# Kernel tuning notes

Hardware: AMD Instinct MI355X
Metric: run time of the kernel (lower is better)

## Reference

```python
import jax, jax.numpy as jnp
import numpy as np

HIDDEN = 1024
HEADS = 16
HEAD_DIM = 64
B, S = 4, 2048


def setup_inputs() -> dict:
    key = jax.random.key(0)
    ks = jax.random.split(key, 7)
    sd = 1.0 / np.sqrt(HIDDEN)
    inp = {
        "inputs": jax.random.normal(ks[0], (B, S, HIDDEN), dtype=jnp.float32),
        "Wq": jax.random.normal(ks[1], (HIDDEN, HEADS * HEAD_DIM), dtype=jnp.float32) * sd,
        "bq": jnp.zeros((HEADS * HEAD_DIM,), dtype=jnp.float32),
        "Wk": jax.random.normal(ks[2], (HIDDEN, HEADS * HEAD_DIM), dtype=jnp.float32) * sd,
        "bk": jnp.zeros((HEADS * HEAD_DIM,), dtype=jnp.float32),
        "Wv": jax.random.normal(ks[3], (HIDDEN, HEADS * HEAD_DIM), dtype=jnp.float32) * sd,
        "bv": jnp.zeros((HEADS * HEAD_DIM,), dtype=jnp.float32),
        "attention_mask": jnp.zeros((B, 1, 1, S), dtype=jnp.float32),
        "attention_head_size": HEAD_DIM,
    }
    return inp


def _rope_tables(seq_len, head_dim, dtype):
    # embeddings[n, d] with interleaved sin/cos layout: [s0, c0, s1, c1, ...]
    pos = jnp.arange(seq_len, dtype=jnp.float32)
    inv_freq = jnp.power(10000.0, -2.0 * jnp.arange(head_dim // 2, dtype=jnp.float32) / head_dim)
    ang = pos[:, None] * inv_freq[None, :]                      # [S, D/2]
    emb = jnp.stack([jnp.sin(ang), jnp.cos(ang)], axis=-1).reshape(seq_len, head_dim)
    cos_pos = jnp.repeat(emb[:, 1::2], 2, axis=-1).astype(dtype)  # [S, D]
    sin_pos = jnp.repeat(emb[:, 0::2], 2, axis=-1).astype(dtype)  # [S, D]
    return cos_pos[None, None], sin_pos[None, None]               # [1,1,S,D]


def _rotate(x):
    # stack([-x_odd, x_even], -1).reshape: interleaved rotate-half
    x2 = jnp.stack([-x[..., 1::2], x[..., 0::2]], axis=-1)
    return x2.reshape(x.shape)


def reference(inputs, Wq, bq, Wk, bk, Wv, bv, attention_mask, attention_head_size):
    Bq, Sq, _ = inputs.shape
    H = HEADS
    D = attention_head_size
    all_head = H * D

    def proj(W, b):
        y = inputs @ W + b                              # [B,S,H*D]
        return y.reshape(Bq, Sq, H, D).transpose(0, 2, 1, 3)  # [B,H,S,D]

    q = proj(Wq, bq)
    k = proj(Wk, bk)
    v = proj(Wv, bv)

    cos_pos, sin_pos = _rope_tables(Sq, D, inputs.dtype)
    q = q * cos_pos + _rotate(q) * sin_pos
    k = k * cos_pos + _rotate(k) * sin_pos

    # NOTE: module scales by sqrt(all_head_size), not sqrt(head_dim)
    scores = jnp.einsum("bhqd,bhkd->bhqk", q, k) / jnp.sqrt(jnp.float32(all_head)).astype(inputs.dtype)
    scores = scores + attention_mask
    probs = jax.nn.softmax(scores, axis=-1)
    ctx = jnp.einsum("bhqk,bhkd->bhqd", probs, v)       # [B,H,S,D]
    ctx = ctx.transpose(0, 2, 1, 3).reshape(Bq, Sq, all_head)
    return ctx, q, k
```

## Files before the change

kernel.cpp:

```cpp
#include <hip/hip_runtime.h>


#define B_  4
#define S_  2048
#define H_  16
#define D_  64
#define HID 1024
#define M_  (B_ * S_)

typedef __attribute__((ext_vector_type(8))) short    bf16x8;
typedef __attribute__((ext_vector_type(4))) float    f32x4;
typedef __attribute__((ext_vector_type(4))) unsigned short u16x4;
typedef __attribute__((ext_vector_type(8))) unsigned short u16x8;
typedef __attribute__((ext_vector_type(2))) unsigned u32x2;

__device__ __forceinline__ unsigned short f2bf(float f) {
    union { float f; unsigned u; } v; v.f = f;
    unsigned r = v.u + 0x7fffu + ((v.u >> 16) & 1u);
    return (unsigned short)(r >> 16);
}

__device__ __forceinline__ void async16(const unsigned short* g, unsigned short* l) {
    __builtin_amdgcn_global_load_lds(
        (const __attribute__((address_space(1))) void*)g,
        (__attribute__((address_space(3))) void*)l, 16, 0, 0);
}

__global__ __launch_bounds__(256) void rope_table_kernel(float* __restrict__ tab)
{
    int i = blockIdx.x * 256 + threadIdx.x;
    int s = i >> 6, d = i & 63;
    const float NEG_LN1E4_32 = -0.28782313662425576f;
    float freq = __expf(NEG_LN1E4_32 * (float)(d >> 1));
    float ang = (float)s * freq;
    tab[i]          = cosf(ang);
    tab[131072 + i] = sinf(ang);
}

__global__ __launch_bounds__(256) void cast_x_kernel(
    const float* __restrict__ X, unsigned short* __restrict__ Xb)
{
    int i = (blockIdx.x * 256 + threadIdx.x) * 4;
    float4 v = *(const float4*)(X + i);
    u16x4 o;
    o[0] = f2bf(v.x); o[1] = f2bf(v.y); o[2] = f2bf(v.z); o[3] = f2bf(v.w);
    *(u16x4*)(Xb + i) = o;
}

__global__ __launch_bounds__(256) void cast_wt_kernel(
    const float* __restrict__ Wq, const float* __restrict__ Wk,
    const float* __restrict__ Wv, unsigned short* __restrict__ Wt)
{
    __shared__ float tile[64][65];
    int z = blockIdx.z;
    const float* W = (z == 0) ? Wq : ((z == 1) ? Wk : Wv);
    unsigned short* out = Wt + (size_t)z * HID * HID;
    int n0 = blockIdx.x * 64, k0 = blockIdx.y * 64;
    int tx = threadIdx.x & 63, ty0 = threadIdx.x >> 6;
#pragma unroll
    for (int i = 0; i < 16; i++) {
        int ty = ty0 * 16 + i;
        tile[ty][tx] = W[(size_t)(k0 + ty) * HID + n0 + tx];
    }
    __syncthreads();
#pragma unroll
    for (int i = 0; i < 16; i++) {
        int ty = ty0 * 16 + i;
        out[(size_t)(n0 + ty) * HID + k0 + tx] = f2bf(tile[tx][ty]);
    }
}

#define BM 128
#define BN 128
#define BKQ 32

__global__ __launch_bounds__(256) void qkv_gemm_kernel(
    const unsigned short* __restrict__ Xb, const unsigned short* __restrict__ Wt,
    const float* __restrict__ bq, const float* __restrict__ bk,
    const float* __restrict__ bv,
    const float* __restrict__ cosT, const float* __restrict__ sinT,
    float* out,
    unsigned short* __restrict__ Qb, unsigned short* __restrict__ Kb,
    unsigned short* __restrict__ Vb)
{
    __shared__ unsigned short As[BM * BKQ];
    __shared__ unsigned short Bs[BN * BKQ];

    const size_t Q_OFF = (size_t)B_ * S_ * HID;
    const size_t K_OFF = 2 * Q_OFF;

    int z = blockIdx.z;
    const unsigned short* W = Wt + (size_t)z * HID * HID;
    const float* bias = (z == 0) ? bq : ((z == 1) ? bk : bv);

    int n0 = blockIdx.x * BN, m0 = blockIdx.y * BM;
    int tid = threadIdx.x;
    int wave = tid >> 6, lane = tid & 63;
    int quad = lane >> 4, l15 = lane & 15;
    int wm = (wave >> 1) * 64;
    int wn = (wave & 1) * 64;

    const unsigned short* Ag = Xb + (size_t)m0 * HID;
    const unsigned short* Bg = W  + (size_t)n0 * HID;

    int e0 = tid, e1 = 256 + tid;
    int r0 = e0 >> 2, c0 = (e0 & 3) * 8;
    int r1 = e1 >> 2, c1 = (e1 & 3) * 8;

    f32x4 acc[4][4] = {};

    for (int k0 = 0; k0 < HID; k0 += BKQ) {
        async16(Ag + (size_t)r0 * HID + k0 + c0, &As[e0 * 8]);
        async16(Ag + (size_t)r1 * HID + k0 + c1, &As[e1 * 8]);
        async16(Bg + (size_t)r0 * HID + k0 + c0, &Bs[e0 * 8]);
        async16(Bg + (size_t)r1 * HID + k0 + c1, &Bs[e1 * 8]);
        __syncthreads();

        bf16x8 af[4], bf[4];
#pragma unroll
        for (int t = 0; t < 4; t++)
            af[t] = *(const bf16x8*)&As[(wm + t * 16 + l15) * BKQ + quad * 8];
#pragma unroll
        for (int t = 0; t < 4; t++)
            bf[t] = *(const bf16x8*)&Bs[(wn + t * 16 + l15) * BKQ + quad * 8];
#pragma unroll
        for (int rt = 0; rt < 4; rt++)
#pragma unroll
            for (int ct = 0; ct < 4; ct++)
                acc[rt][ct] = __builtin_amdgcn_mfma_f32_16x16x32_bf16(
                    af[rt], bf[ct], acc[rt][ct], 0, 0, 0);
        __syncthreads();
    }

#pragma unroll
    for (int ct = 0; ct < 4; ct++) {
        int n = n0 + wn + ct * 16 + l15;
        float bval = bias[n];
        int h = n >> 6, d = n & 63;
#pragma unroll
        for (int rt = 0; rt < 4; rt++) {
#pragma unroll
            for (int r = 0; r < 4; r++) {
                int m = m0 + wm + rt * 16 + quad * 4 + r;
                int b = m >> 11, s = m & (S_ - 1);
                float y = acc[rt][ct][r] + bval;
                size_t o = ((size_t)(b * H_ + h) * S_ + s) * D_ + d;
                if (z < 2) {
                    float c  = cosT[s * 64 + d];
                    float sn = sinT[s * 64 + d];
                    float p = __shfl_xor(y, 1);
                    float yr = ((d & 1) == 0) ? (y * c - p * sn) : (y * c + p * sn);
                    if (z == 0) { out[Q_OFF + o] = yr; Qb[o] = f2bf(yr); }
                    else        { out[K_OFF + o] = yr; Kb[o] = f2bf(yr); }
                } else {
                    Vb[o] = f2bf(y);
                }
            }
        }
    }
}

__global__ __launch_bounds__(256) void transpose_v_kernel(
    const unsigned short* __restrict__ Vb, unsigned short* __restrict__ Vt)
{
    __shared__ unsigned short t[64][72];
    int bh = blockIdx.y;
    int s0 = blockIdx.x * 64;
    const unsigned short* src = Vb + ((size_t)bh * S_ + s0) * D_;
    unsigned short* dst = Vt + (size_t)bh * D_ * S_;
    int tid = threadIdx.x;
#pragma unroll
    for (int i = 0; i < 2; i++) {
        int e = i * 256 + tid;
        int row = e >> 3, c = (e & 7) * 8;
        u16x8 v = *(const u16x8*)(src + (size_t)row * D_ + c);
#pragma unroll
        for (int j = 0; j < 8; j++) t[row][c + j] = v[j];
    }
    __syncthreads();
#pragma unroll
    for (int i = 0; i < 2; i++) {
        int e = i * 256 + tid;
        int d = e >> 3, sc = (e & 7) * 8;
        u16x8 v;
#pragma unroll
        for (int j = 0; j < 8; j++) v[j] = t[sc + j][d];
        *(u16x8*)(dst + (size_t)d * S_ + s0 + sc) = v;
    }
}

#define TR 72

__global__ __launch_bounds__(256, 4) void attn_kernel(
    const unsigned short* __restrict__ Qb, const unsigned short* __restrict__ Kb,
    const unsigned short* __restrict__ Vt, const float* __restrict__ mask,
    float* __restrict__ out)
{
    __shared__ union {
        struct {
            unsigned short Ks[2][64 * TR];
            unsigned short Vs[2][64 * TR];
        } s;
        float oT[4][2][16][68];
    } u;

    int h  = blockIdx.x;
    int qt = blockIdx.y;
    int b  = blockIdx.z;
    int tid = threadIdx.x;
    int wave = tid >> 6, lane = tid & 63;
    int quad = lane >> 4, l15 = lane & 15;

    size_t bh = (size_t)(b * H_ + h);
    const unsigned short* Qp = Qb + bh * S_ * D_;
    const unsigned short* Kp = Kb + bh * S_ * D_;
    const unsigned short* Vp = Vt + bh * D_ * S_;
    const float* mp = mask + (size_t)b * S_;

    bf16x8 qb[2][2];
#pragma unroll
    for (int qg = 0; qg < 2; qg++)
#pragma unroll
        for (int hf = 0; hf < 2; hf++) {
            int qrow = qt * 128 + qg * 64 + wave * 16 + l15;
            qb[qg][hf] = *(const bf16x8*)(Qp + (size_t)qrow * D_ + hf * 32 + quad * 8);
        }

    f32x4 o[2][4] = {};
    float psum[2] = {0.0f, 0.0f};
    const float C2    = 0.03125f * 1.44269504f;
    const float LOG2E = 1.44269504f;

    int sr0 = tid >> 3, sg0 = (tid & 7) * 8;
    int sr1 = sr0 + 32;

    u16x8 kr0 = *(const u16x8*)(Kp + (size_t)sr0 * D_ + sg0);
    u16x8 kr1 = *(const u16x8*)(Kp + (size_t)sr1 * D_ + sg0);
    u16x8 vr0 = *(const u16x8*)(Vp + (size_t)sr0 * S_ + sg0);
    u16x8 vr1 = *(const u16x8*)(Vp + (size_t)sr1 * S_ + sg0);

    int cur = 0;
    for (int kv0 = 0; kv0 < S_; kv0 += 64) {
        *(u16x8*)&u.s.Ks[cur][sr0 * TR + sg0] = kr0;
        *(u16x8*)&u.s.Ks[cur][sr1 * TR + sg0] = kr1;
        *(u16x8*)&u.s.Vs[cur][sr0 * TR + sg0] = vr0;
        *(u16x8*)&u.s.Vs[cur][sr1 * TR + sg0] = vr1;
        __syncthreads();

        int kvn = (kv0 + 64 < S_) ? kv0 + 64 : 0;
        kr0 = *(const u16x8*)(Kp + (size_t)(kvn + sr0) * D_ + sg0);
        kr1 = *(const u16x8*)(Kp + (size_t)(kvn + sr1) * D_ + sg0);
        vr0 = *(const u16x8*)(Vp + (size_t)sr0 * S_ + kvn + sg0);
        vr1 = *(const u16x8*)(Vp + (size_t)sr1 * S_ + kvn + sg0);

        const unsigned short* Ksc = u.s.Ks[cur];
        const unsigned short* Vsc = u.s.Vs[cur];

        f32x4 sa[2][4] = {};
        __builtin_amdgcn_s_setprio(1);
#pragma unroll
        for (int mt = 0; mt < 4; mt++) {
            bf16x8 kf0 = *(const bf16x8*)&Ksc[(mt * 16 + l15) * TR + quad * 8];
            bf16x8 kf1 = *(const bf16x8*)&Ksc[(mt * 16 + l15) * TR + 32 + quad * 8];
#pragma unroll
            for (int qg = 0; qg < 2; qg++) {
                sa[qg][mt] = __builtin_amdgcn_mfma_f32_16x16x32_bf16(kf0, qb[qg][0], sa[qg][mt], 0, 0, 0);
                sa[qg][mt] = __builtin_amdgcn_mfma_f32_16x16x32_bf16(kf1, qb[qg][1], sa[qg][mt], 0, 0, 0);
            }
        }
        __builtin_amdgcn_s_setprio(0);

        unsigned pw[2][4][2];
#pragma unroll
        for (int mt = 0; mt < 4; mt++) {
            f32x4 mkv = *(const f32x4*)(mp + kv0 + mt * 16 + quad * 4);
#pragma unroll
            for (int qg = 0; qg < 2; qg++) {
                f32x4 pv;
#pragma unroll
                for (int r = 0; r < 4; r++)
                    pv[r] = exp2f(sa[qg][mt][r] * C2 + mkv[r] * LOG2E);
                psum[qg] += (pv[0] + pv[1]) + (pv[2] + pv[3]);
                asm("v_cvt_pk_bf16_f32 %0, %1, %2"
                    : "=v"(pw[qg][mt][0]) : "v"(pv[0]), "v"(pv[1]));
                asm("v_cvt_pk_bf16_f32 %0, %1, %2"
                    : "=v"(pw[qg][mt][1]) : "v"(pv[2]), "v"(pv[3]));
            }
        }

        bf16x8 pb[2][2];
#pragma unroll
        for (int qg = 0; qg < 2; qg++)
#pragma unroll
            for (int hf = 0; hf < 2; hf++) {
                union { unsigned w[4]; bf16x8 v; } pbu;
#pragma unroll
                for (int t = 0; t < 2; t++) {
                    unsigned A = pw[qg][2 * hf + 0][t];
                    unsigned B = pw[qg][2 * hf + 1][t];
                    u32x2 r1 = __builtin_amdgcn_permlane32_swap(A, B, false, false);
                    u32x2 r2 = __builtin_amdgcn_permlane16_swap(r1[0], r1[1], false, false);
                    pbu.w[t]     = r2[0];
                    pbu.w[2 + t] = r2[1];
                }
                pb[qg][hf] = pbu.v;
            }

        __builtin_amdgcn_s_setprio(1);
#pragma unroll
        for (int ct = 0; ct < 4; ct++) {
            bf16x8 vf0 = *(const bf16x8*)&Vsc[(ct * 16 + l15) * TR + quad * 8];
            bf16x8 vf1 = *(const bf16x8*)&Vsc[(ct * 16 + l15) * TR + 32 + quad * 8];
#pragma unroll
            for (int qg = 0; qg < 2; qg++) {
                o[qg][ct] = __builtin_amdgcn_mfma_f32_16x16x32_bf16(vf0, pb[qg][0], o[qg][ct], 0, 0, 0);
                o[qg][ct] = __builtin_amdgcn_mfma_f32_16x16x32_bf16(vf1, pb[qg][1], o[qg][ct], 0, 0, 0);
            }
        }
        __builtin_amdgcn_s_setprio(0);

        cur ^= 1;
    }
    __syncthreads();

#pragma unroll
    for (int qg = 0; qg < 2; qg++) {
        psum[qg] += __shfl_xor(psum[qg], 16);
        psum[qg] += __shfl_xor(psum[qg], 32);
    }

#pragma unroll
    for (int qg = 0; qg < 2; qg++) {
        float inv = 1.0f / psum[qg];
#pragma unroll
        for (int ct = 0; ct < 4; ct++) {
            float4 vv;
            vv.x = o[qg][ct][0] * inv; vv.y = o[qg][ct][1] * inv;
            vv.z = o[qg][ct][2] * inv; vv.w = o[qg][ct][3] * inv;
            *(float4*)&u.oT[wave][qg][l15][ct * 16 + quad * 4] = vv;
        }
    }
    __builtin_amdgcn_wave_barrier();
    {
        int qq = lane >> 2, d0 = (lane & 3) * 16;
#pragma unroll
        for (int qg = 0; qg < 2; qg++) {
            int s_abs = qt * 128 + qg * 64 + wave * 16 + qq;
            float* dst = out + ((size_t)b * S_ + s_abs) * (H_ * D_) + h * D_ + d0;
#pragma unroll
            for (int j = 0; j < 4; j++) {
                float4 vj = *(float4*)&u.oT[wave][qg][qq][d0 + j * 4];
                *(float4*)(dst + j * 4) = vj;
            }
        }
    }
}

extern "C" void kernel_launch(void* const* d_in, const int* in_sizes, int n_in,
                              void* d_out, int out_size, void* d_ws, size_t ws_size,
                              hipStream_t stream)
{
    const float* X    = (const float*)d_in[0];
    const float* Wq   = (const float*)d_in[1];
    const float* bq   = (const float*)d_in[2];
    const float* Wk   = (const float*)d_in[3];
    const float* bk   = (const float*)d_in[4];
    const float* Wv   = (const float*)d_in[5];
    const float* bv   = (const float*)d_in[6];
    const float* mask = (const float*)d_in[7];

    char* ws = (char*)d_ws;
    unsigned short* Xb = (unsigned short*)(ws);
    unsigned short* Wt = (unsigned short*)(ws + 16777216);
    unsigned short* Qb = (unsigned short*)(ws + 23068672);
    unsigned short* Kb = (unsigned short*)(ws + 39845888);
    unsigned short* Vb = (unsigned short*)(ws + 56623104);
    unsigned short* Vt = Xb;

    float* tab = (float*)d_out;

    rope_table_kernel<<<dim3(131072 / 256), 256, 0, stream>>>(tab);
    cast_x_kernel<<<dim3(M_ * HID / 4 / 256), 256, 0, stream>>>(X, Xb);
    cast_wt_kernel<<<dim3(16, 16, 3), 256, 0, stream>>>(Wq, Wk, Wv, Wt);
    qkv_gemm_kernel<<<dim3(HID / BN, M_ / BM, 3), 256, 0, stream>>>(
        Xb, Wt, bq, bk, bv, tab, tab + 131072, (float*)d_out, Qb, Kb, Vb);
    transpose_v_kernel<<<dim3(S_ / 64, B_ * H_), 256, 0, stream>>>(Vb, Vt);
    attn_kernel<<<dim3(H_, S_ / 128, B_), 256, 0, stream>>>(
        Qb, Kb, Vt, mask, (float*)d_out);
}
```

Measured before the change: 399.0 us.

## Compute softmax row sums via MFMA with ones, use raw v_exp, prefetch mask and V

Replaces the per-lane VALU accumulation of softmax denominators with an extra MFMA against a ones vector, so the row sum comes out of the matrix unit using the same bf16-rounded probabilities that feed the PV product. It also swaps exp2f for the raw v_exp_f32 instruction, register-prefetches the next tile's mask values alongside the K/V loads, and software-pipelines the V fragment LDS reads one column tile ahead. The goal is to cut VALU work and latency in the softmax stage, at the cost of extra MFMAs, more registers, and reduced exp precision and denormal handling.

```diff
diff --git a/kernel.cpp b/kernel.cpp
--- a/kernel.cpp
+++ b/kernel.cpp
@@ -24,6 +24,12 @@
     __builtin_amdgcn_global_load_lds(
         (const __attribute__((address_space(1))) void*)g,
         (__attribute__((address_space(3))) void*)l, 16, 0, 0);
+}
+
+__device__ __forceinline__ float fast_exp2(float x) {
+    float r;
+    asm("v_exp_f32 %0, %1" : "=v"(r) : "v"(x));
+    return r;
 }
 
 __global__ __launch_bounds__(256) void rope_table_kernel(float* __restrict__ tab)
@@ -227,9 +233,16 @@
         }
 
     f32x4 o[2][4] = {};
-    float psum[2] = {0.0f, 0.0f};
+    f32x4 acc1[2] = {};
     const float C2    = 0.03125f * 1.44269504f;
     const float LOG2E = 1.44269504f;
+
+    bf16x8 ones_af;
+    {
+        short o1 = (l15 == 0) ? (short)0x3F80 : (short)0;
+#pragma unroll
+        for (int j = 0; j < 8; j++) ones_af[j] = o1;
+    }
 
     int sr0 = tid >> 3, sg0 = (tid & 7) * 8;
     int sr1 = sr0 + 32;
@@ -238,6 +251,10 @@
     u16x8 kr1 = *(const u16x8*)(Kp + (size_t)sr1 * D_ + sg0);
     u16x8 vr0 = *(const u16x8*)(Vp + (size_t)sr0 * S_ + sg0);
     u16x8 vr1 = *(const u16x8*)(Vp + (size_t)sr1 * S_ + sg0);
+    f32x4 mk[4];
+#pragma unroll
+    for (int mt = 0; mt < 4; mt++)
+        mk[mt] = *(const f32x4*)(mp + mt * 16 + quad * 4);
 
     int cur = 0;
     for (int kv0 = 0; kv0 < S_; kv0 += 64) {
@@ -252,6 +269,10 @@
         kr1 = *(const u16x8*)(Kp + (size_t)(kvn + sr1) * D_ + sg0);
         vr0 = *(const u16x8*)(Vp + (size_t)sr0 * S_ + kvn + sg0);
         vr1 = *(const u16x8*)(Vp + (size_t)sr1 * S_ + kvn + sg0);
+        f32x4 mkn[4];
+#pragma unroll
+        for (int mt = 0; mt < 4; mt++)
+            mkn[mt] = *(const f32x4*)(mp + kvn + mt * 16 + quad * 4);
 
         const unsigned short* Ksc = u.s.Ks[cur];
         const unsigned short* Vsc = u.s.Vs[cur];
@@ -270,23 +291,26 @@
         }
         __builtin_amdgcn_s_setprio(0);
 
+        bf16x8 vf0 = *(const bf16x8*)&Vsc[l15 * TR + quad * 8];
+        bf16x8 vf1 = *(const bf16x8*)&Vsc[l15 * TR + 32 + quad * 8];
+
         unsigned pw[2][4][2];
 #pragma unroll
         for (int mt = 0; mt < 4; mt++) {
-            f32x4 mkv = *(const f32x4*)(mp + kv0 + mt * 16 + quad * 4);
 #pragma unroll
             for (int qg = 0; qg < 2; qg++) {
                 f32x4 pv;
 #pragma unroll
                 for (int r = 0; r < 4; r++)
-                    pv[r] = exp2f(sa[qg][mt][r] * C2 + mkv[r] * LOG2E);
-                psum[qg] += (pv[0] + pv[1]) + (pv[2] + pv[3]);
+                    pv[r] = fast_exp2(sa[qg][mt][r] * C2 + mk[mt][r] * LOG2E);
                 asm("v_cvt_pk_bf16_f32 %0, %1, %2"
                     : "=v"(pw[qg][mt][0]) : "v"(pv[0]), "v"(pv[1]));
                 asm("v_cvt_pk_bf16_f32 %0, %1, %2"
                     : "=v"(pw[qg][mt][1]) : "v"(pv[2]), "v"(pv[3]));
             }
         }
+#pragma unroll
+        for (int mt = 0; mt < 4; mt++) mk[mt] = mkn[mt];
 
         bf16x8 pb[2][2];
 #pragma unroll
@@ -309,13 +333,22 @@
         __builtin_amdgcn_s_setprio(1);
 #pragma unroll
         for (int ct = 0; ct < 4; ct++) {
-            bf16x8 vf0 = *(const bf16x8*)&Vsc[(ct * 16 + l15) * TR + quad * 8];
-            bf16x8 vf1 = *(const bf16x8*)&Vsc[(ct * 16 + l15) * TR + 32 + quad * 8];
+            bf16x8 nf0, nf1;
+            if (ct < 3) {
+                nf0 = *(const bf16x8*)&Vsc[((ct + 1) * 16 + l15) * TR + quad * 8];
+                nf1 = *(const bf16x8*)&Vsc[((ct + 1) * 16 + l15) * TR + 32 + quad * 8];
+            }
 #pragma unroll
             for (int qg = 0; qg < 2; qg++) {
                 o[qg][ct] = __builtin_amdgcn_mfma_f32_16x16x32_bf16(vf0, pb[qg][0], o[qg][ct], 0, 0, 0);
                 o[qg][ct] = __builtin_amdgcn_mfma_f32_16x16x32_bf16(vf1, pb[qg][1], o[qg][ct], 0, 0, 0);
             }
+            if (ct < 3) { vf0 = nf0; vf1 = nf1; }
+        }
+#pragma unroll
+        for (int qg = 0; qg < 2; qg++) {
+            acc1[qg] = __builtin_amdgcn_mfma_f32_16x16x32_bf16(ones_af, pb[qg][0], acc1[qg], 0, 0, 0);
+            acc1[qg] = __builtin_amdgcn_mfma_f32_16x16x32_bf16(ones_af, pb[qg][1], acc1[qg], 0, 0, 0);
         }
         __builtin_amdgcn_s_setprio(0);
 
@@ -323,11 +356,10 @@
     }
     __syncthreads();
 
-#pragma unroll
-    for (int qg = 0; qg < 2; qg++) {
-        psum[qg] += __shfl_xor(psum[qg], 16);
-        psum[qg] += __shfl_xor(psum[qg], 32);
-    }
+    float psum[2];
+#pragma unroll
+    for (int qg = 0; qg < 2; qg++)
+        psum[qg] = __shfl(acc1[qg][0], l15);
 
 #pragma unroll
     for (int qg = 0; qg < 2; qg++) {
```

Measured after the change: 803.6 us. 2.01x slower.
